# Performance work log

Measured on AMD Instinct MI355X. Metric: run time of the kernel, lower is better.

The kernel has to match this reference:

```python
import jax, jax.numpy as jnp
import numpy as np

B, S, E = 2, 1024, 768
H, D = 12, 64          # num_heads, head_dim
M = 768                # mlp_hidden_size
Q = 4                  # q_stride
EPS = 1e-5


def _layernorm(x, w, b):
    mu = x.mean(-1, keepdims=True)
    var = ((x - mu) ** 2).mean(-1, keepdims=True)
    return (x - mu) * jax.lax.rsqrt(var + EPS) * w + b


def setup_inputs() -> dict:
    key = jax.random.key(0)
    ks = jax.random.split(key, 16)
    s = 0.02
    d = {
        'x': jax.random.normal(ks[0], (B, S, E), jnp.float32),
        'ln1_w': jnp.ones((E,), jnp.float32), 'ln1_b': jnp.zeros((E,), jnp.float32),
        'Wq': jax.random.normal(ks[1], (E, E), jnp.float32) * s, 'bq': jnp.zeros((E,), jnp.float32),
        'Wk': jax.random.normal(ks[2], (E, E), jnp.float32) * s, 'bk': jnp.zeros((E,), jnp.float32),
        'Wv': jax.random.normal(ks[3], (E, E), jnp.float32) * s, 'bv': jnp.zeros((E,), jnp.float32),
        'Wo': jax.random.normal(ks[4], (E, E), jnp.float32) * s, 'bo': jnp.zeros((E,), jnp.float32),
        'pond': jnp.zeros((), jnp.float32),  # ponderation_param
        'ln2_w': jnp.ones((E,), jnp.float32), 'ln2_b': jnp.zeros((E,), jnp.float32),
        'fc1_W': jax.random.normal(ks[5], (Q * M, E), jnp.float32) * s, 'fc1_b': jnp.zeros((Q * M,), jnp.float32),
        'vqc_W': jax.random.normal(ks[6], (M, M), jnp.float32) * s, 'vqc_b': jnp.zeros((M,), jnp.float32),
        'fc2_W': jax.random.normal(ks[7], (E, Q * M), jnp.float32) * s, 'fc2_b': jnp.zeros((E,), jnp.float32),
    }
    return d


def reference(x, ln1_w, ln1_b, Wq, bq, Wk, bk, Wv, bv, Wo, bo, pond,
              ln2_w, ln2_b, fc1_W, fc1_b, vqc_W, vqc_b, fc2_W, fc2_b):
    # --- attention sublayer ---
    h = _layernorm(x, ln1_w, ln1_b)
    def heads(W, b):
        return (h @ W.T + b).reshape(B, S, H, D).transpose(0, 2, 1, 3)  # [B,H,S,D]
    q, k, v = heads(Wq, bq), heads(Wk, bk), heads(Wv, bv)

    # N=2: einsum with identity A reduces to q k^T
    logits = jnp.einsum('bhid,bhjd->bhij', q, k) / jnp.sqrt(jnp.float32(D))
    attn = jax.nn.softmax(logits, axis=-1)  # dropout is identity at inference

    # RBF similarity blending ('linear' ponderation)
    q_norm = (q ** 2).sum(-1, keepdims=True)                  # [B,H,S,1]
    k_norm = (k ** 2).sum(-1, keepdims=True).swapaxes(-2, -1)  # [B,H,1,S]
    d2 = jnp.maximum(q_norm + k_norm - 2.0 * jnp.einsum('bhid,bhjd->bhij', q, k), 0.0)
    sigma2 = jnp.clip(q_norm, 1e-8, 1e4)
    rbf = jnp.exp(-d2 / sigma2)
    rbf = rbf / jnp.maximum(rbf.sum(-1, keepdims=True), 1e-8)
    rbf = jnp.nan_to_num(rbf, nan=0.0, posinf=0.0, neginf=0.0)
    s_val = jax.nn.sigmoid(pond)
    p0, p1 = 1.0 - s_val, s_val
    attn = (p0 * attn + p1 * rbf) / (p0 + p1 + 1e-7)

    vals = jnp.einsum('bhij,bhjd->bhid', attn, v)
    vals = vals.transpose(0, 2, 1, 3).reshape(B, S, E)
    x = x + (vals @ Wo.T + bo)

    # --- sliced MLP sublayer (q_stride=4, overlapping offset-1 slices) ---
    y = _layernorm(x, ln2_w, ln2_b)
    h1 = y @ fc1_W.T + fc1_b                                  # [B,S,Q*M]
    slices = jnp.stack([h1[:, :, i:i + M] for i in range(Q)], axis=2)  # [B,S,Q,M]
    z = slices @ vqc_W.T + vqc_b                              # vqc (linear fallback)
    z = z.transpose(0, 1, 3, 2).reshape(B, S, Q * M)          # permute(0,1,3,2).view
    z = jax.nn.gelu(z, approximate=False)
    out = z @ fc2_W.T + fc2_b
    return x + out
```

## Files before the change

kernel.cpp:

```cpp
#include <hip/hip_runtime.h>
#include <math.h>

#define E_DIM 768
#define S_LEN 1024
#define B_SZ 2
#define H_CNT 12
#define D_HEAD 64
#define M_DIM 768
#define Q_STRIDE 4
#define N_FC1 771

typedef __attribute__((ext_vector_type(8))) short bf16x8;
typedef __attribute__((ext_vector_type(4))) float f32x4;

#define AS1 __attribute__((address_space(1)))
#define AS3 __attribute__((address_space(3)))

__device__ __forceinline__ void gld_lds16(void* lds, const void* g) {
    __builtin_amdgcn_global_load_lds((const AS1 void*)g, (AS3 void*)lds, 16, 0, 0);
}

__device__ __forceinline__ short f2bf(float f) {
    unsigned u = __float_as_uint(f);
    unsigned r = (u + 0x7fffu + ((u >> 16) & 1u)) >> 16;
    return (short)r;
}

__device__ __forceinline__ float bf2f(short s) {
    return __uint_as_float(((unsigned)(unsigned short)s) << 16);
}


__device__ __forceinline__ float block_reduce_sum(float v, volatile float* red) {
#pragma unroll
    for (int off = 32; off > 0; off >>= 1) v += __shfl_xor(v, off);
    __syncthreads();
    if ((threadIdx.x & 63) == 0) red[threadIdx.x >> 6] = v;
    __syncthreads();
    return red[0] + red[1] + red[2] + red[3];
}


__global__ __launch_bounds__(256) void preamble(
        const float* __restrict__ Wq, const float* __restrict__ Wk,
        const float* __restrict__ Wv, const float* __restrict__ Wo,
        const float* __restrict__ fc1W, const float* __restrict__ vqcW,
        const float* __restrict__ fc2W, short* __restrict__ dst,
        const float* __restrict__ bq, const float* __restrict__ bk,
        const float* __restrict__ bv, float* __restrict__ bqkv,
        const float* __restrict__ x, const float* __restrict__ ln1_w,
        const float* __restrict__ ln1_b, short* __restrict__ actb) {
    __shared__ float red[4];
    int tid = threadIdx.x;
    if (blockIdx.x < 2048) {
        int row = blockIdx.x;
        const float* xr = x + (size_t)row * E_DIM;
        float v0 = xr[tid], v1 = xr[tid + 256], v2 = xr[tid + 512];
        float s = block_reduce_sum(v0 + v1 + v2, red);
        float mu = s * (1.0f / E_DIM);
        float d0 = v0 - mu, d1 = v1 - mu, d2 = v2 - mu;
        float var = block_reduce_sum(d0 * d0 + d1 * d1 + d2 * d2, red) * (1.0f / E_DIM);
        float rs = rsqrtf(var + 1e-5f);
        short* orow = actb + (size_t)row * E_DIM;
        orow[tid]       = f2bf(d0 * rs * ln1_w[tid]       + ln1_b[tid]);
        orow[tid + 256] = f2bf(d1 * rs * ln1_w[tid + 256] + ln1_b[tid + 256]);
        orow[tid + 512] = f2bf(d2 * rs * ln1_w[tid + 512] + ln1_b[tid + 512]);
        return;
    }
    if (blockIdx.x == 2048) {
#pragma unroll
        for (int u = 0; u < 9; u++) {
            int i = tid + u * 256;
            float v = (i < 768) ? bq[i] : (i < 1536) ? bk[i - 768] : bv[i - 1536];
            bqkv[i] = v;
        }
        return;
    }
    int t = (blockIdx.x - 2049) * 256 + tid;
    if (t >= 1475136) return;
    int e = t * 4;
    const float* src; int off;
    if      (e < 589824)  { src = Wq;   off = e; }
    else if (e < 1179648) { src = Wk;   off = e - 589824; }
    else if (e < 1769472) { src = Wv;   off = e - 1179648; }
    else if (e < 2359296) { src = Wo;   off = e - 1769472; }
    else if (e < 2951424) { src = fc1W; off = e - 2359296; }
    else if (e < 3541248) { src = vqcW; off = e - 2951424; }
    else                  { src = fc2W; off = e - 3541248; }
    float4 v = *(const float4*)(src + off);
    short4 o = make_short4(f2bf(v.x), f2bf(v.y), f2bf(v.z), f2bf(v.w));
    *(short4*)(dst + e) = o;
}


template <int OUTMODE, int MR>
__global__ __launch_bounds__(256, 2) void gemm_bf16(
        const short* __restrict__ A, int lda,
        const short* __restrict__ W, int ldw,
        const float* __restrict__ bias,
        void* __restrict__ outp, int ldo, size_t spitch,
        short* __restrict__ Kfp, short* __restrict__ Vfp,
        int N, int klen, int dogelu,
        float* __restrict__ qnG, float* __restrict__ knG) {
    constexpr int MI = MR / 32;
    constexpr int AH = MR * 32;
    constexpr int NA = MR / 64;
    constexpr int ASL = 2 * AH;
    __shared__ short At[2 * ASL];
    __shared__ short Bt[2 * 8192];
    const int tid = threadIdx.x;
    const int lane = tid & 63;
    const int wave = tid >> 6;
    const int wr = (wave >> 1) * (MI * 16);
    const int wc = (wave & 1) * 64;
    const int ml = lane & 15;
    const int kq = lane >> 4;
    const int row0 = blockIdx.y * MR;
    const int col0 = blockIdx.x * 128;
    const int kbase = blockIdx.z * klen;

    const short* Ag[NA]; int aoff[NA];
#pragma unroll
    for (int u = 0; u < NA; u++) {
        int c = tid + u * 256;
        int am = c >> 2, ak = ((c & 3) ^ ((am >> 1) & 3)) * 8;
        Ag[u] = A + (size_t)(row0 + am) * lda + ak + kbase;
        aoff[u] = c * 8;
    }
    const int c0 = tid, c1 = tid + 256;
    const int bm0 = c0 >> 2, bk0 = (((c0 & 3) ^ ((bm0 >> 1) & 3))) * 8;
    const int bm1 = c1 >> 2, bk1 = (((c1 & 3) ^ ((bm1 >> 1) & 3))) * 8;
    int wrow0 = col0 + bm0; if (wrow0 > N - 1) wrow0 = N - 1;
    int wrow1 = col0 + bm1; if (wrow1 > N - 1) wrow1 = N - 1;
    const short* Wg0 = W + (size_t)wrow0 * ldw + bk0 + kbase;
    const short* Wg1 = W + (size_t)wrow1 * ldw + bk1 + kbase;

    const int kxor = (kq ^ ((ml >> 1) & 3)) * 8;

    f32x4 acc[MI][4];
#pragma unroll
    for (int i = 0; i < MI; i++)
#pragma unroll
        for (int j = 0; j < 4; j++) acc[i][j] = {0.f, 0.f, 0.f, 0.f};

    auto stage = [&](int buf, int k0) {
        short* Ab = At + buf * ASL;
        short* Bb = Bt + buf * 8192;
#pragma unroll
        for (int u = 0; u < NA; u++) {
            gld_lds16(Ab + aoff[u], Ag[u] + k0);
            gld_lds16(Ab + AH + aoff[u], Ag[u] + k0 + 32);
        }
        gld_lds16(Bb + c0 * 8, Wg0 + k0);
        gld_lds16(Bb + c1 * 8, Wg1 + k0);
        gld_lds16(Bb + 4096 + c0 * 8, Wg0 + k0 + 32);
        gld_lds16(Bb + 4096 + c1 * 8, Wg1 + k0 + 32);
    };

    stage(0, 0);
    int cur = 0;
    for (int k0 = 0; k0 < klen; k0 += 64) {
        __syncthreads();
        if (k0 + 64 < klen) stage(cur ^ 1, k0 + 64);
        const short* Ac = At + cur * ASL;
        const short* Bc = Bt + cur * 8192;
#pragma unroll
        for (int half = 0; half < 2; half++) {
            const short* Ah = Ac + half * AH;
            const short* Bh = Bc + half * 4096;
            bf16x8 af[MI], bfr[4];
#pragma unroll
            for (int i = 0; i < MI; i++)
                af[i] = *(const bf16x8*)&Ah[(wr + i * 16 + ml) * 32 + kxor];
#pragma unroll
            for (int j = 0; j < 4; j++)
                bfr[j] = *(const bf16x8*)&Bh[(wc + j * 16 + ml) * 32 + kxor];
#pragma unroll
            for (int i = 0; i < MI; i++)
#pragma unroll
                for (int j = 0; j < 4; j++)
                    acc[i][j] = __builtin_amdgcn_mfma_f32_16x16x32_bf16(af[i], bfr[j], acc[i][j], 0, 0, 0);
        }
        cur ^= 1;
    }

    float sq[MI][4];
    if constexpr (OUTMODE == 3) {
#pragma unroll
        for (int i = 0; i < MI; i++)
#pragma unroll
            for (int rr = 0; rr < 4; rr++) sq[i][rr] = 0.f;
    }
#pragma unroll
    for (int i = 0; i < MI; i++) {
#pragma unroll
        for (int j = 0; j < 4; j++) {
#pragma unroll
            for (int rr = 0; rr < 4; rr++) {
                int r = row0 + wr + i * 16 + kq * 4 + rr;
                int c = col0 + wc + j * 16 + ml;
                if (c < N) {
                    float v = acc[i][j][rr];
                    if (OUTMODE < 4) v += bias[c];
                    if (OUTMODE == 2 && dogelu)
                        v = 0.5f * v * (1.0f + erff(v * 0.70710678118654752f));
                    if (OUTMODE == 2) {
                        ((short*)outp)[(size_t)(r >> 2) * ldo + c * 4 + (r & 3)] = f2bf(v);
                    } else if (OUTMODE == 5) {
                        ((short*)outp)[blockIdx.z * spitch + (size_t)r * ldo + c] = f2bf(v);
                    } else if (OUTMODE == 3) {
                        sq[i][rr] += v * v;
                        int s = r & 1023, bb = r >> 10;
                        if (c < 768) {
                            ((short*)outp)[(size_t)r * 768 + c] = f2bf(v);
                        } else if (c < 1536) {
                            int df = c - 768; int hh = df >> 6, d = df & 63;
                            int bh2 = bb * 12 + hh;
                            size_t idx = ((size_t)(bh2 * 64 + (s >> 4)) * 2 + (d >> 5)) * 512
                                       + (size_t)((d >> 3) & 3) * 128 + (size_t)(s & 15) * 8 + (d & 7);
                            Kfp[idx] = f2bf(v);
                        } else {
                            int df = c - 1536; int hh = df >> 6, d = df & 63;
                            int bh2 = bb * 12 + hh;
                            size_t idx = ((size_t)(bh2 * 32 + (s >> 5))) * 2048
                                       + (size_t)(d >> 4) * 512 + (size_t)((s >> 3) & 3) * 128
                                       + (size_t)(d & 15) * 8 + (s & 7);
                            Vfp[idx] = f2bf(v);
                        }
                    }
                }
            }
        }
    }

    if constexpr (OUTMODE == 3) {
        int cb = col0 + wc;
        if (cb < 1536) {
            float* dst = (cb < 768) ? qnG : knG;
            int hh = ((cb < 768) ? cb : cb - 768) >> 6;
#pragma unroll
            for (int i = 0; i < MI; i++) {
#pragma unroll
                for (int rr = 0; rr < 4; rr++) {
                    float s = sq[i][rr];
                    s += __shfl_xor(s, 1);
                    s += __shfl_xor(s, 2);
                    s += __shfl_xor(s, 4);
                    s += __shfl_xor(s, 8);
                    if (ml == 0) {
                        int r = row0 + wr + i * 16 + kq * 4 + rr;
                        int bb = r >> 10, sidx = r & 1023;
                        dst[(size_t)(bb * 12 + hh) * 1024 + sidx] = s;
                    }
                }
            }
        }
    }
}


__global__ __launch_bounds__(256) void reduce_wo_ln(
        const short* __restrict__ part, const float* __restrict__ bo,
        const float* __restrict__ x, const float* __restrict__ w,
        const float* __restrict__ bvec, float* __restrict__ x2,
        short* __restrict__ y) {
    __shared__ float red[4];
    int row = blockIdx.x, tid = threadIdx.x;
    const size_t SP = (size_t)2048 * 768;
    const short* pr = part + (size_t)row * 768;
    const float* xr = x + (size_t)row * 768;
    float* x2r = x2 + (size_t)row * 768;
    float v[3];
#pragma unroll
    for (int u = 0; u < 3; u++) {
        int c = tid + u * 256;
        float s = bo[c] + xr[c];
#pragma unroll
        for (int z = 0; z < 4; z++) s += bf2f(pr[z * SP + c]);
        v[u] = s; x2r[c] = s;
    }
    float s = block_reduce_sum(v[0] + v[1] + v[2], red);
    float mu = s * (1.0f / 768.f);
    float d0 = v[0] - mu, d1 = v[1] - mu, d2 = v[2] - mu;
    float var = block_reduce_sum(d0 * d0 + d1 * d1 + d2 * d2, red) * (1.0f / 768.f);
    float rs = rsqrtf(var + 1e-5f);
    short* orow = y + (size_t)row * 768;
    orow[tid]       = f2bf(d0 * rs * w[tid]       + bvec[tid]);
    orow[tid + 256] = f2bf(d1 * rs * w[tid + 256] + bvec[tid + 256]);
    orow[tid + 512] = f2bf(d2 * rs * w[tid + 512] + bvec[tid + 512]);
}

__global__ __launch_bounds__(256) void reduce_fc1_expand(
        const short* __restrict__ part, const float* __restrict__ b,
        const short* __restrict__ y, const short* __restrict__ w768,
        short* __restrict__ Avqc) {
    __shared__ float row[772];
    __shared__ float red[4];
    int r = blockIdx.x, tid = threadIdx.x;
    const size_t SP = (size_t)2048 * 768;
    const short* pr = part + (size_t)r * 768;
#pragma unroll
    for (int u = 0; u < 3; u++) {
        int c = tid + u * 256;
        float s = b[c];
#pragma unroll
        for (int z = 0; z < 4; z++) s += bf2f(pr[z * SP + c]);
        row[c] = s;
    }
    const short* yr = y + (size_t)r * 768;
    float y0 = bf2f(yr[tid]), y1 = bf2f(yr[tid + 256]), y2 = bf2f(yr[tid + 512]);
#pragma unroll
    for (int k = 0; k < 3; k++) {
        const short* wk = w768 + k * 768;
        float s = y0 * bf2f(wk[tid]) + y1 * bf2f(wk[tid + 256]) + y2 * bf2f(wk[tid + 512]);
        s = block_reduce_sum(s, red);
        if (tid == 0) row[768 + k] = s + b[768 + k];
    }
    __syncthreads();
#pragma unroll
    for (int q = 0; q < 4; q++) {
        short* orow = Avqc + (size_t)(r * 4 + q) * 768;
#pragma unroll
        for (int u = 0; u < 3; u++) {
            int m = tid + u * 256;
            orow[m] = f2bf(row[m + q]);
        }
    }
}

__global__ __launch_bounds__(256) void reduce_fc2(
        const short* __restrict__ part, const float* __restrict__ b,
        const float* __restrict__ x2, float* __restrict__ out) {
    int t = blockIdx.x * 256 + threadIdx.x;
    int row = t / 192;
    int c = (t - row * 192) * 4;
    size_t off = (size_t)row * 768 + c;
    const size_t SP = (size_t)2048 * 768;
    float4 bb = *(const float4*)(b + c);
    float4 xx = *(const float4*)(x2 + off);
    float o0 = bb.x + xx.x, o1 = bb.y + xx.y, o2 = bb.z + xx.z, o3 = bb.w + xx.w;
#pragma unroll
    for (int z = 0; z < 4; z++) {
        short4 v = *(const short4*)(part + z * SP + off);
        o0 += bf2f(v.x); o1 += bf2f(v.y); o2 += bf2f(v.z); o3 += bf2f(v.w);
    }
    float4 o = make_float4(o0, o1, o2, o3);
    *(float4*)(out + off) = o;
}


__global__ __launch_bounds__(256) void attn_mfma(
        const short* __restrict__ Qb,
        const short* __restrict__ Kf,
        const short* __restrict__ Vf,
        const float* __restrict__ pond,
        const float* __restrict__ qnG,
        const float* __restrict__ knG,
        short* __restrict__ vals) {
    __shared__ __align__(16) short Kt[2 * 4096];
    __shared__ __align__(16) short Vt[2 * 4096];
    __shared__ float esx[2][16], rsx[2][16];
    __shared__ __align__(16) short Pe[4 * 16 * 72];
    __shared__ __align__(16) short Pr[4 * 16 * 72];

    const int tid = threadIdx.x;
    const int lane = tid & 63;
    const int wave = tid >> 6;
    const int wq = wave & 1;
    const int wp = wave >> 1;
    const int ml = lane & 15;
    const int kq = lane >> 4;

    const int fid = blockIdx.x;
    const int w = (fid & 7) * 96 + (fid >> 3);
    const int qt2 = w & 31;
    const int bh = w >> 5;
    const int b = (bh >= 12) ? 1 : 0;
    const int h = bh - b * 12;

    const int qrow = b * S_LEN + qt2 * 32 + wq * 16 + ml;
    const short* qp = Qb + (size_t)qrow * 768 + h * 64 + kq * 8;
    bf16x8 aq0 = *(const bf16x8*)qp;
    bf16x8 aq1 = *(const bf16x8*)(qp + 32);

    const float* qnB = qnG + (size_t)bh * 1024 + qt2 * 32 + wq * 16;
    float qn_r[4], is_r[4];
#pragma unroll
    for (int r = 0; r < 4; r++) {
        qn_r[r] = qnB[kq * 4 + r];
        is_r[r] = 1.0f / fminf(fmaxf(qn_r[r], 1e-8f), 1e4f);
    }
    const float* knB = knG + (size_t)bh * 1024;

    f32x4 Oe[4], Or[4];
#pragma unroll
    for (int dt = 0; dt < 4; dt++) { Oe[dt] = {0.f,0.f,0.f,0.f}; Or[dt] = {0.f,0.f,0.f,0.f}; }
    float es_p[4] = {0.f,0.f,0.f,0.f}, rs_p[4] = {0.f,0.f,0.f,0.f};

    const short* KfB = Kf + (size_t)bh * 65536;
    const short* VfB = Vf + (size_t)bh * 65536;
    short* PeW = Pe + wave * 1152;
    short* PrW = Pr + wave * 1152;
    const short* KtW = Kt + wp * 4096;
    const short* VtW = Vt + wp * 4096;

    for (int it = 0; it < 8; it++) {
        __syncthreads();
        {
            const short* sk0 = KfB + it * 4096 + tid * 8;
            gld_lds16(Kt + tid * 8, sk0);
            gld_lds16(Kt + 2048 + tid * 8, sk0 + 2048);
            const short* sk1 = KfB + (it + 8) * 4096 + tid * 8;
            gld_lds16(Kt + 4096 + tid * 8, sk1);
            gld_lds16(Kt + 6144 + tid * 8, sk1 + 2048);
            const short* sv0 = VfB + it * 4096 + tid * 8;
            gld_lds16(Vt + tid * 8, sv0);
            gld_lds16(Vt + 2048 + tid * 8, sv0 + 2048);
            const short* sv1 = VfB + (it + 8) * 4096 + tid * 8;
            gld_lds16(Vt + 4096 + tid * 8, sv1);
            gld_lds16(Vt + 6144 + tid * 8, sv1 + 2048);
        }
        float knt[4];
        {
            const float* knI = knB + (it + 8 * wp) * 64 + ml;
#pragma unroll
            for (int jtl = 0; jtl < 4; jtl++) knt[jtl] = knI[jtl * 16];
        }
        __syncthreads();

#pragma unroll
        for (int jtl = 0; jtl < 4; jtl++) {
            bf16x8 bk0 = *(const bf16x8*)&KtW[(jtl * 2 + 0) * 512 + lane * 8];
            bf16x8 bk1 = *(const bf16x8*)&KtW[(jtl * 2 + 1) * 512 + lane * 8];
            f32x4 c = {0.f,0.f,0.f,0.f};
            c = __builtin_amdgcn_mfma_f32_16x16x32_bf16(aq0, bk0, c, 0, 0, 0);
            c = __builtin_amdgcn_mfma_f32_16x16x32_bf16(aq1, bk1, c, 0, 0, 0);
#pragma unroll
            for (int r = 0; r < 4; r++) {
                float qk = c[r];
                float e = __expf(qk * 0.125f);
                float tt = (2.f * qk - qn_r[r] - knt[jtl]) * is_r[r];
                float rb = fminf(__expf(tt), 1.0f);
                es_p[r] += e; rs_p[r] += rb;
                PeW[(kq * 4 + r) * 72 + jtl * 16 + ml] = f2bf(e);
                PrW[(kq * 4 + r) * 72 + jtl * 16 + ml] = f2bf(rb);
            }
        }

#pragma unroll
        for (int jcl = 0; jcl < 2; jcl++) {
            bf16x8 pa_e = *(const bf16x8*)&PeW[ml * 72 + jcl * 32 + kq * 8];
            bf16x8 pa_r = *(const bf16x8*)&PrW[ml * 72 + jcl * 32 + kq * 8];
#pragma unroll
            for (int dt = 0; dt < 4; dt++) {
                bf16x8 bv = *(const bf16x8*)&VtW[(jcl * 4 + dt) * 512 + lane * 8];
                Oe[dt] = __builtin_amdgcn_mfma_f32_16x16x32_bf16(pa_e, bv, Oe[dt], 0, 0, 0);
                Or[dt] = __builtin_amdgcn_mfma_f32_16x16x32_bf16(pa_r, bv, Or[dt], 0, 0, 0);
            }
        }
    }

#pragma unroll
    for (int off = 1; off <= 8; off <<= 1) {
#pragma unroll
        for (int r = 0; r < 4; r++) {
            es_p[r] += __shfl_xor(es_p[r], off);
            rs_p[r] += __shfl_xor(rs_p[r], off);
        }
    }

    __syncthreads();
    float* cb = (float*)Kt;
    if (wp == 1) {
        float* cl = cb + (size_t)(wq * 64 + lane) * 32;
#pragma unroll
        for (int dt = 0; dt < 4; dt++)
#pragma unroll
            for (int r = 0; r < 4; r++) {
                cl[dt * 4 + r] = Oe[dt][r];
                cl[16 + dt * 4 + r] = Or[dt][r];
            }
        if (ml == 0) {
#pragma unroll
            for (int r = 0; r < 4; r++) {
                esx[wq][kq * 4 + r] = es_p[r];
                rsx[wq][kq * 4 + r] = rs_p[r];
            }
        }
    }
    __syncthreads();
    if (wp == 0) {
        float p = pond[0];
        float sv = 1.0f / (1.0f + __expf(-p));
        float p0 = 1.0f - sv, p1 = sv;
        float blendinv = 1.0f / (p0 + p1 + 1e-7f);
        const float* cl = cb + (size_t)(wq * 64 + lane) * 32;
        float we[4], wr[4];
#pragma unroll
        for (int r = 0; r < 4; r++) {
            float es = es_p[r] + esx[wq][kq * 4 + r];
            float rs = rs_p[r] + rsx[wq][kq * 4 + r];
            we[r] = p0 * blendinv / es;
            wr[r] = p1 * blendinv / fmaxf(rs, 1e-8f);
        }
#pragma unroll
        for (int dt = 0; dt < 4; dt++) {
#pragma unroll
            for (int r = 0; r < 4; r++) {
                float oe = Oe[dt][r] + cl[dt * 4 + r];
                float orr = Or[dt][r] + cl[16 + dt * 4 + r];
                float v = oe * we[r] + orr * wr[r];
                int token = b * S_LEN + qt2 * 32 + wq * 16 + kq * 4 + r;
                vals[(size_t)token * 768 + h * 64 + dt * 16 + ml] = f2bf(v);
            }
        }
    }
}


extern "C" void kernel_launch(void* const* d_in, const int* in_sizes, int n_in,
                              void* d_out, int out_size, void* d_ws, size_t ws_size,
                              hipStream_t stream) {
    const float* x     = (const float*)d_in[0];
    const float* ln1_w = (const float*)d_in[1];
    const float* ln1_b = (const float*)d_in[2];
    const float* Wq    = (const float*)d_in[3];
    const float* bq    = (const float*)d_in[4];
    const float* Wk    = (const float*)d_in[5];
    const float* bk    = (const float*)d_in[6];
    const float* Wv    = (const float*)d_in[7];
    const float* bv    = (const float*)d_in[8];
    const float* Wo    = (const float*)d_in[9];
    const float* bo    = (const float*)d_in[10];
    const float* pond  = (const float*)d_in[11];
    const float* ln2_w = (const float*)d_in[12];
    const float* ln2_b = (const float*)d_in[13];
    const float* fc1_W = (const float*)d_in[14];
    const float* fc1_b = (const float*)d_in[15];
    const float* vqc_W = (const float*)d_in[16];
    const float* vqc_b = (const float*)d_in[17];
    const float* fc2_W = (const float*)d_in[18];
    const float* fc2_b = (const float*)d_in[19];
    float* out = (float*)d_out;

    char* p = (char*)d_ws;
    short* Qb   = (short*)p;  p += (size_t)2048 * 768 * 2;
    short* Kfb  = (short*)p;  p += (size_t)2048 * 768 * 2;
    short* Vfb  = (short*)p;  p += (size_t)2048 * 768 * 2;
    float* x2   = (float*)p;  p += (size_t)2048 * 768 * 4;
    float* bqkv = (float*)p;  p += 2304 * 4;
    float* qnG  = (float*)p;  p += (size_t)24 * 1024 * 4;
    float* knG  = (float*)p;  p += (size_t)24 * 1024 * 4;
    short* actb = (short*)p;  p += (size_t)2048 * 768 * 2;
    short* g    = (short*)p;  p += (size_t)2048 * 3072 * 2;
    short* Avqc = (short*)p;  p += (size_t)8192 * 768 * 2;
    short* partb = (short*)p; p += (size_t)4 * 2048 * 768 * 2;
    short* wreg = (short*)p;  p += (size_t)5900544 * 2;
    short* Wqkvb = wreg;
    short* Wob   = wreg + 1769472;
    short* fc1b  = wreg + 2359296;
    short* vqcb  = wreg + 2951424;
    short* fc2b  = wreg + 3541248;

    dim3 blk(256);
    const size_t SP = (size_t)2048 * 768;

    preamble<<<7812, blk, 0, stream>>>(Wq, Wk, Wv, Wo, fc1_W, vqc_W, fc2_W, wreg,
                                       bq, bk, bv, bqkv, x, ln1_w, ln1_b, actb);
    gemm_bf16<3, 64><<<dim3(18, 32, 1), blk, 0, stream>>>(actb, 768, Wqkvb, 768, bqkv,
                                                          Qb, 768, 0, Kfb, Vfb, 2304, 768, 0,
                                                          qnG, knG);
    attn_mfma<<<768, blk, 0, stream>>>(Qb, Kfb, Vfb, pond, qnG, knG, actb);
    gemm_bf16<5, 64><<<dim3(6, 32, 4), blk, 0, stream>>>(actb, 768, Wob, 768, nullptr,
                                                         partb, 768, SP,
                                                         nullptr, nullptr, 768, 192, 0,
                                                         nullptr, nullptr);
    reduce_wo_ln<<<2048, blk, 0, stream>>>(partb, bo, x, ln2_w, ln2_b, x2, actb);
    gemm_bf16<5, 64><<<dim3(6, 32, 4), blk, 0, stream>>>(actb, 768, fc1b, 768, nullptr,
                                                         partb, 768, SP,
                                                         nullptr, nullptr, 768, 192, 0,
                                                         nullptr, nullptr);
    reduce_fc1_expand<<<2048, blk, 0, stream>>>(partb, fc1_b, actb, fc1b + 768 * 768, Avqc);
    gemm_bf16<2, 64><<<dim3(6, 128, 1), blk, 0, stream>>>(Avqc, 768, vqcb, 768, vqc_b,
                                                          g, 3072, 0, nullptr, nullptr, 768, 768, 1,
                                                          nullptr, nullptr);
    gemm_bf16<5, 64><<<dim3(6, 32, 4), blk, 0, stream>>>(g, 3072, fc2b, 3072, nullptr,
                                                         partb, 768, SP,
                                                         nullptr, nullptr, 768, 768, 0,
                                                         nullptr, nullptr);
    reduce_fc2<<<1536, blk, 0, stream>>>(partb, fc2_b, x2, out);
}
```

Baseline: 150.3 us.

## Double-buffer K/V tiles in attention kernel with smaller per-step chunks

Restructures the attention loop from 8 iterations over 64-key chunks into 16 iterations over 32-key chunks per wave pair. K/V tiles are double-buffered in LDS, so the next tile's global-to-LDS load is issued before the current tile is computed, replacing the two barriers per iteration with one. The partial-accumulator exchange buffer also changes to a transposed layout, which should reduce LDS bank conflicts. The cost is more loop iterations with fewer MFMAs each, and correctness depends on the async LDS loads finishing before the next barrier.

```diff
diff --git a/kernel.cpp b/kernel.cpp
--- a/kernel.cpp
+++ b/kernel.cpp
@@ -357,11 +357,11 @@
         const float* __restrict__ qnG,
         const float* __restrict__ knG,
         short* __restrict__ vals) {
-    __shared__ __align__(16) short Kt[2 * 4096];
-    __shared__ __align__(16) short Vt[2 * 4096];
+    __shared__ __align__(16) short Kt[8192];
+    __shared__ __align__(16) short Vt[8192];
     __shared__ float esx[2][16], rsx[2][16];
-    __shared__ __align__(16) short Pe[4 * 16 * 72];
-    __shared__ __align__(16) short Pr[4 * 16 * 72];
+    __shared__ __align__(16) short Pe[4 * 16 * 40];
+    __shared__ __align__(16) short Pr[4 * 16 * 40];
 
     const int tid = threadIdx.x;
     const int lane = tid & 63;
@@ -390,7 +390,7 @@
         qn_r[r] = qnB[kq * 4 + r];
         is_r[r] = 1.0f / fminf(fmaxf(qn_r[r], 1e-8f), 1e4f);
     }
-    const float* knB = knG + (size_t)bh * 1024;
+    const float* knB = knG + (size_t)bh * 1024 + wp * 512;
 
     f32x4 Oe[4], Or[4];
 #pragma unroll
@@ -399,39 +399,33 @@
 
     const short* KfB = Kf + (size_t)bh * 65536;
     const short* VfB = Vf + (size_t)bh * 65536;
-    short* PeW = Pe + wave * 1152;
-    short* PrW = Pr + wave * 1152;
-    const short* KtW = Kt + wp * 4096;
-    const short* VtW = Vt + wp * 4096;
-
-    for (int it = 0; it < 8; it++) {
+    short* PeW = Pe + wave * 640;
+    short* PrW = Pr + wave * 640;
+
+    auto stage = [&](int buf, int t) {
+        gld_lds16(Kt + buf * 4096 + tid * 8,        KfB + (size_t)(4 * t) * 512 + tid * 8);
+        gld_lds16(Kt + buf * 4096 + 2048 + tid * 8, KfB + (size_t)(64 + 4 * t) * 512 + tid * 8);
+        gld_lds16(Vt + buf * 4096 + tid * 8,        VfB + (size_t)t * 2048 + tid * 8);
+        gld_lds16(Vt + buf * 4096 + 2048 + tid * 8, VfB + (size_t)(16 + t) * 2048 + tid * 8);
+    };
+
+    stage(0, 0);
+    int cur = 0;
+    for (int t = 0; t < 16; t++) {
         __syncthreads();
-        {
-            const short* sk0 = KfB + it * 4096 + tid * 8;
-            gld_lds16(Kt + tid * 8, sk0);
-            gld_lds16(Kt + 2048 + tid * 8, sk0 + 2048);
-            const short* sk1 = KfB + (it + 8) * 4096 + tid * 8;
-            gld_lds16(Kt + 4096 + tid * 8, sk1);
-            gld_lds16(Kt + 6144 + tid * 8, sk1 + 2048);
-            const short* sv0 = VfB + it * 4096 + tid * 8;
-            gld_lds16(Vt + tid * 8, sv0);
-            gld_lds16(Vt + 2048 + tid * 8, sv0 + 2048);
-            const short* sv1 = VfB + (it + 8) * 4096 + tid * 8;
-            gld_lds16(Vt + 4096 + tid * 8, sv1);
-            gld_lds16(Vt + 6144 + tid * 8, sv1 + 2048);
-        }
-        float knt[4];
-        {
-            const float* knI = knB + (it + 8 * wp) * 64 + ml;
-#pragma unroll
-            for (int jtl = 0; jtl < 4; jtl++) knt[jtl] = knI[jtl * 16];
-        }
-        __syncthreads();
-
-#pragma unroll
-        for (int jtl = 0; jtl < 4; jtl++) {
+        if (t + 1 < 16) stage(cur ^ 1, t + 1);
+
+        const float* knI = knB + t * 32 + ml;
+        float kn0 = knI[0], kn1 = knI[16];
+
+        const short* KtW = Kt + cur * 4096 + wp * 2048;
+        const short* VtW = Vt + cur * 4096 + wp * 2048;
+
+#pragma unroll
+        for (int jtl = 0; jtl < 2; jtl++) {
             bf16x8 bk0 = *(const bf16x8*)&KtW[(jtl * 2 + 0) * 512 + lane * 8];
             bf16x8 bk1 = *(const bf16x8*)&KtW[(jtl * 2 + 1) * 512 + lane * 8];
+            float knt = jtl ? kn1 : kn0;
             f32x4 c = {0.f,0.f,0.f,0.f};
             c = __builtin_amdgcn_mfma_f32_16x16x32_bf16(aq0, bk0, c, 0, 0, 0);
             c = __builtin_amdgcn_mfma_f32_16x16x32_bf16(aq1, bk1, c, 0, 0, 0);
@@ -439,25 +433,23 @@
             for (int r = 0; r < 4; r++) {
                 float qk = c[r];
                 float e = __expf(qk * 0.125f);
-                float tt = (2.f * qk - qn_r[r] - knt[jtl]) * is_r[r];
+                float tt = (2.f * qk - qn_r[r] - knt) * is_r[r];
                 float rb = fminf(__expf(tt), 1.0f);
                 es_p[r] += e; rs_p[r] += rb;
-                PeW[(kq * 4 + r) * 72 + jtl * 16 + ml] = f2bf(e);
-                PrW[(kq * 4 + r) * 72 + jtl * 16 + ml] = f2bf(rb);
+                PeW[(kq * 4 + r) * 40 + jtl * 16 + ml] = f2bf(e);
+                PrW[(kq * 4 + r) * 40 + jtl * 16 + ml] = f2bf(rb);
             }
         }
 
-#pragma unroll
-        for (int jcl = 0; jcl < 2; jcl++) {
-            bf16x8 pa_e = *(const bf16x8*)&PeW[ml * 72 + jcl * 32 + kq * 8];
-            bf16x8 pa_r = *(const bf16x8*)&PrW[ml * 72 + jcl * 32 + kq * 8];
-#pragma unroll
-            for (int dt = 0; dt < 4; dt++) {
-                bf16x8 bv = *(const bf16x8*)&VtW[(jcl * 4 + dt) * 512 + lane * 8];
-                Oe[dt] = __builtin_amdgcn_mfma_f32_16x16x32_bf16(pa_e, bv, Oe[dt], 0, 0, 0);
-                Or[dt] = __builtin_amdgcn_mfma_f32_16x16x32_bf16(pa_r, bv, Or[dt], 0, 0, 0);
-            }
-        }
+        bf16x8 pa_e = *(const bf16x8*)&PeW[ml * 40 + kq * 8];
+        bf16x8 pa_r = *(const bf16x8*)&PrW[ml * 40 + kq * 8];
+#pragma unroll
+        for (int dt = 0; dt < 4; dt++) {
+            bf16x8 bv = *(const bf16x8*)&VtW[dt * 512 + lane * 8];
+            Oe[dt] = __builtin_amdgcn_mfma_f32_16x16x32_bf16(pa_e, bv, Oe[dt], 0, 0, 0);
+            Or[dt] = __builtin_amdgcn_mfma_f32_16x16x32_bf16(pa_r, bv, Or[dt], 0, 0, 0);
+        }
+        cur ^= 1;
     }
 
 #pragma unroll
@@ -472,13 +464,13 @@
     __syncthreads();
     float* cb = (float*)Kt;
     if (wp == 1) {
-        float* cl = cb + (size_t)(wq * 64 + lane) * 32;
+        float* cl = cb + wq * 64 + lane;
 #pragma unroll
         for (int dt = 0; dt < 4; dt++)
 #pragma unroll
             for (int r = 0; r < 4; r++) {
-                cl[dt * 4 + r] = Oe[dt][r];
-                cl[16 + dt * 4 + r] = Or[dt][r];
+                cl[(dt * 4 + r) * 128] = Oe[dt][r];
+                cl[(16 + dt * 4 + r) * 128] = Or[dt][r];
             }
         if (ml == 0) {
 #pragma unroll
@@ -494,7 +486,6 @@
         float sv = 1.0f / (1.0f + __expf(-p));
         float p0 = 1.0f - sv, p1 = sv;
         float blendinv = 1.0f / (p0 + p1 + 1e-7f);
-        const float* cl = cb + (size_t)(wq * 64 + lane) * 32;
         float we[4], wr[4];
 #pragma unroll
         for (int r = 0; r < 4; r++) {
@@ -507,8 +498,9 @@
         for (int dt = 0; dt < 4; dt++) {
 #pragma unroll
             for (int r = 0; r < 4; r++) {
-                float oe = Oe[dt][r] + cl[dt * 4 + r];
-                float orr = Or[dt][r] + cl[16 + dt * 4 + r];
+                int e0 = dt * 4 + r;
+                float oe = Oe[dt][r] + cb[e0 * 128 + wq * 64 + lane];
+                float orr = Or[dt][r] + cb[(16 + e0) * 128 + wq * 64 + lane];
                 float v = oe * we[r] + orr * wr[r];
                 int token = b * S_LEN + qt2 * 32 + wq * 16 + kq * 4 + r;
                 vals[(size_t)token * 768 + h * 64 + dt * 16 + ml] = f2bf(v);
```

New measurement: 151.5 us. No clear change (+0.8%).
